# Optimization experiments

Hardware: AMD Instinct MI355X
Metric: run time of the kernel (lower is better)

Reference implementation:

```python
import jax, jax.numpy as jnp
import numpy as np

N = 50000        # nodes
E = 800000       # edges (avg degree 16)
IN_DIM = 256
H = 8            # heads
D = 32           # out_dim per head
T = 4            # edge_type_num
F = 16           # edge_feature_dim
NEG_SLOPE = 0.2


def setup_inputs() -> dict:
    key = jax.random.key(0)
    ks = jax.random.split(key, 9)
    feat = jax.random.normal(ks[0], (N, IN_DIM), dtype=jnp.float32)
    e_pro = jax.random.normal(ks[1], (E, F), dtype=jnp.float32)
    mask = jax.random.uniform(ks[2], (E, T), dtype=jnp.float32)
    W_n = jax.random.normal(ks[3], (IN_DIM, H * D), dtype=jnp.float32) * (1.0 / np.sqrt(IN_DIM))
    attn_l = jax.random.normal(ks[4], (H, D, T), dtype=jnp.float32) * 0.1
    attn_r = jax.random.normal(ks[5], (H, D, T), dtype=jnp.float32) * 0.1
    attn_m = jax.random.normal(ks[6], (H, F, T), dtype=jnp.float32) * 0.1
    src = jax.random.randint(ks[7], (E,), 0, N, dtype=jnp.int32)
    dst = jax.random.randint(ks[8], (E,), 0, N, dtype=jnp.int32)
    return {"feat": feat, "e_pro": e_pro, "mask": mask, "W_n": W_n,
            "attn_l": attn_l, "attn_r": attn_r, "attn_m": attn_m,
            "src": src, "dst": dst}


def reference(feat, e_pro, mask, W_n, attn_l, attn_r, attn_m, src, dst):
    # node projection: [N, H, D]
    feat_src = (feat @ W_n).reshape(N, H, D)

    # per-node attention logits per edge type: [N, H, T]
    el = jnp.einsum("nhd,hdt->nht", feat_src, attn_l)
    er = jnp.einsum("nhd,hdt->nht", feat_src, attn_r)
    # per-edge logits per edge type: [E, H, T]
    em = jnp.einsum("ef,hft->eht", e_pro, attn_m)

    # bmm with edge-type mask [E, T] -> scalar per head: [E, H]
    left = jnp.einsum("eht,et->eh", el[src], mask)
    right = jnp.einsum("eht,et->eh", er[dst], mask)
    em_e = jnp.einsum("eht,et->eh", em, mask)

    e = (left + right + em_e) / 3.0
    e = jnp.where(e > 0, e, NEG_SLOPE * e)  # leaky_relu

    # edge softmax over incoming edges of each dst node (stable)
    e_max = jax.ops.segment_max(e, dst, num_segments=N)          # [N, H]
    e_exp = jnp.exp(e - e_max[dst])                               # [E, H]
    e_sum = jax.ops.segment_sum(e_exp, dst, num_segments=N)      # [N, H]
    a = e_exp / e_sum[dst]                                       # [E, H]

    # u_mul_e + sum aggregation: [E, H, D] -> [N, H, D]
    msg = feat_src[src] * a[:, :, None]
    rst = jax.ops.segment_sum(msg, dst, num_segments=N)

    # cat=True: concat heads
    return rst.reshape(N, H * D)
```

## Files before the change

kernel.cpp:

```cpp
#include <hip/hip_runtime.h>
#include <hip/hip_bf16.h>
#include <hip/hip_fp16.h>

#define NN 50000
#define NEDGE 800000
#define INDIM 256
#define NH 8
#define ND 32
#define HD 256
#define NT 4
#define NF 16

typedef __attribute__((ext_vector_type(8))) short s16x8;
typedef __attribute__((ext_vector_type(4))) float f32x4;
typedef unsigned short u16;

__device__ __forceinline__ float bf2f(u16 u) {
    return __uint_as_float(((unsigned int)u) << 16);
}
__device__ __forceinline__ u16 f2bf(float f) {
    __hip_bfloat16 h = __float2bfloat16(f);
    return *reinterpret_cast<u16*>(&h);
}
__device__ __forceinline__ u16 f2h(float f) {
    __half h = __float2half(f);
    return *reinterpret_cast<u16*>(&h);
}
__device__ __forceinline__ float h2f(u16 u) {
    __half h = *reinterpret_cast<__half*>(&u);
    return __half2float(h);
}

__global__ __launch_bounds__(256) void wt_kernel(const float* __restrict__ W,
                                                 u16* __restrict__ Wt)
{
    int idx = blockIdx.x * 256 + threadIdx.x;
    int k = idx >> 8, c = idx & 255;
    Wt[(size_t)c * 256 + k] = f2bf(W[idx]);
}

__global__ __launch_bounds__(256) void gemm_mfma(
    const float* __restrict__ feat, const u16* __restrict__ Wt,
    u16* __restrict__ fs, int nrows)
{
    const int wave = threadIdx.x >> 6, lane = threadIdx.x & 63;
    const int brow = blockIdx.x * 32;
    const int c0 = wave * 64;
    const int rA = lane & 15;
    const int kg = lane >> 4;

    int r0 = brow + rA;
    int r1 = brow + 16 + rA;
    if (r0 >= nrows) r0 = nrows - 1;
    if (r1 >= nrows) r1 = nrows - 1;

    f32x4 acc[2][4] = {};

    for (int k0 = 0; k0 < 256; k0 += 32) {
        const int kk = k0 + kg * 8;
        const float* pa0 = feat + (size_t)r0 * 256 + kk;
        const float* pa1 = feat + (size_t)r1 * 256 + kk;
        float4 x0 = *reinterpret_cast<const float4*>(pa0);
        float4 x1 = *reinterpret_cast<const float4*>(pa0 + 4);
        float4 y0 = *reinterpret_cast<const float4*>(pa1);
        float4 y1 = *reinterpret_cast<const float4*>(pa1 + 4);
        s16x8 a0, a1;
        a0[0] = (short)f2bf(x0.x); a0[1] = (short)f2bf(x0.y);
        a0[2] = (short)f2bf(x0.z); a0[3] = (short)f2bf(x0.w);
        a0[4] = (short)f2bf(x1.x); a0[5] = (short)f2bf(x1.y);
        a0[6] = (short)f2bf(x1.z); a0[7] = (short)f2bf(x1.w);
        a1[0] = (short)f2bf(y0.x); a1[1] = (short)f2bf(y0.y);
        a1[2] = (short)f2bf(y0.z); a1[3] = (short)f2bf(y0.w);
        a1[4] = (short)f2bf(y1.x); a1[5] = (short)f2bf(y1.y);
        a1[6] = (short)f2bf(y1.z); a1[7] = (short)f2bf(y1.w);
        #pragma unroll
        for (int ct = 0; ct < 4; ++ct) {
            s16x8 b = *reinterpret_cast<const s16x8*>(Wt + (size_t)(c0 + ct * 16 + rA) * 256 + kk);
            acc[0][ct] = __builtin_amdgcn_mfma_f32_16x16x32_bf16(a0, b, acc[0][ct], 0, 0, 0);
            acc[1][ct] = __builtin_amdgcn_mfma_f32_16x16x32_bf16(a1, b, acc[1][ct], 0, 0, 0);
        }
    }

    #pragma unroll
    for (int rt = 0; rt < 2; ++rt) {
        #pragma unroll
        for (int r = 0; r < 4; ++r) {
            int row = brow + rt * 16 + kg * 4 + r;
            if (row < nrows) {
                #pragma unroll
                for (int ct = 0; ct < 4; ++ct) {
                    fs[(size_t)row * 256 + c0 + ct * 16 + rA] = f2bf(acc[rt][ct][r]);
                }
            }
        }
    }
}

__global__ __launch_bounds__(256) void elr_kernel(
    const u16* __restrict__ fs,
    const float* __restrict__ attn_l, const float* __restrict__ attn_r,
    u16* __restrict__ el, u16* __restrict__ er, int n)
{
    __shared__ float s_al[NH * ND * NT];
    __shared__ float s_ar[NH * ND * NT];
    for (int i = threadIdx.x; i < NH * ND * NT; i += 256) {
        s_al[i] = attn_l[i];
        s_ar[i] = attn_r[i];
    }
    __syncthreads();
    int wv = threadIdx.x >> 6, lane = threadIdx.x & 63;
    int node = blockIdx.x * 4 + wv;
    if (node >= n) return;
    int h = lane >> 3, j0 = (lane & 7) * 4;
    ushort4 u = *reinterpret_cast<const ushort4*>(fs + (size_t)node * HD + lane * 4);
    float f0 = bf2f(u.x), f1 = bf2f(u.y), f2 = bf2f(u.z), f3 = bf2f(u.w);
    const float* al = s_al + h * (ND * NT) + j0 * NT;
    const float* ar = s_ar + h * (ND * NT) + j0 * NT;
    float pl[NT], pr[NT];
    #pragma unroll
    for (int t = 0; t < NT; ++t) {
        pl[t] = f0*al[t] + f1*al[NT + t] + f2*al[2*NT + t] + f3*al[3*NT + t];
        pr[t] = f0*ar[t] + f1*ar[NT + t] + f2*ar[2*NT + t] + f3*ar[3*NT + t];
    }
    #pragma unroll
    for (int d = 1; d < 8; d <<= 1) {
        #pragma unroll
        for (int t = 0; t < NT; ++t) {
            pl[t] += __shfl_xor(pl[t], d);
            pr[t] += __shfl_xor(pr[t], d);
        }
    }
    if ((lane & 7) == 0) {
        ushort4 ol, orr;
        ol.x = f2h(pl[0]); ol.y = f2h(pl[1]); ol.z = f2h(pl[2]); ol.w = f2h(pl[3]);
        orr.x = f2h(pr[0]); orr.y = f2h(pr[1]); orr.z = f2h(pr[2]); orr.w = f2h(pr[3]);
        *reinterpret_cast<ushort4*>(el + (size_t)node * (NH*NT) + h * NT) = ol;
        *reinterpret_cast<ushort4*>(er + (size_t)node * (NH*NT) + h * NT) = orr;
    }
}

__global__ void init_kernel(int* cnt, int* cursor, int n) {
    int i = blockIdx.x * 256 + threadIdx.x;
    if (i < n) { cnt[i] = 0; cursor[i] = 0; }
}

__global__ void hist_kernel(const int* __restrict__ dst, int* __restrict__ cnt, int ne) {
    int e = blockIdx.x * 256 + threadIdx.x;
    if (e < ne) atomicAdd(&cnt[dst[e]], 1);
}

__global__ void scan1_kernel(const int* __restrict__ cnt, int* __restrict__ off,
                             int* __restrict__ blksum, int n) {
    __shared__ int sm[256];
    int i = blockIdx.x * 256 + threadIdx.x;
    int v = (i < n) ? cnt[i] : 0;
    sm[threadIdx.x] = v;
    __syncthreads();
    for (int d = 1; d < 256; d <<= 1) {
        int t = (threadIdx.x >= d) ? sm[threadIdx.x - d] : 0;
        __syncthreads();
        sm[threadIdx.x] += t;
        __syncthreads();
    }
    if (i < n) off[i] = sm[threadIdx.x] - v;
    if (threadIdx.x == 255) blksum[blockIdx.x] = sm[255];
}

__global__ void scan2_kernel(int* blksum, int nb) {
    __shared__ int sm[256];
    int v = (threadIdx.x < nb) ? blksum[threadIdx.x] : 0;
    sm[threadIdx.x] = v;
    __syncthreads();
    for (int d = 1; d < 256; d <<= 1) {
        int t = (threadIdx.x >= d) ? sm[threadIdx.x - d] : 0;
        __syncthreads();
        sm[threadIdx.x] += t;
        __syncthreads();
    }
    blksum[threadIdx.x] = sm[threadIdx.x] - v;
}

__global__ void scan3_kernel(int* __restrict__ off, const int* __restrict__ blksum,
                             int n, int ne) {
    int i = blockIdx.x * 256 + threadIdx.x;
    if (i < n) off[i] += blksum[blockIdx.x];
    if (i == 0) off[n] = ne;
}

__global__ __launch_bounds__(256) void edgefill_kernel(
    const float* __restrict__ e_pro, const float* __restrict__ mask,
    const float* __restrict__ attn_m,
    const int* __restrict__ src, const int* __restrict__ dst,
    const u16* __restrict__ el, const u16* __restrict__ er,
    const int* __restrict__ off, int* __restrict__ cursor,
    int* __restrict__ srcS, float* __restrict__ eS, int ne)
{
    __shared__ float s_amT[NF * NT * NH];
    for (int i = threadIdx.x; i < NH * NF * NT; i += 256) {
        int h = i >> 6, f = (i >> 2) & 15, t = i & 3;
        s_amT[(f * NT + t) * NH + h] = attn_m[i];
    }
    __syncthreads();

    int e = blockIdx.x * 32 + (threadIdx.x >> 3);
    if (e >= ne) return;
    const int lane = threadIdx.x & 63;
    const int j = threadIdx.x & 7;

    int s = src[e], d = dst[e];
    float4 mk = *reinterpret_cast<const float4*>(mask + (size_t)e * NT);

    union { uint2 v; u16 u[4]; } lv, rv;
    lv.v = *reinterpret_cast<const uint2*>(el + (size_t)s * (NH*NT) + j * NT);
    rv.v = *reinterpret_cast<const uint2*>(er + (size_t)d * (NH*NT) + j * NT);

    float epf[NF];
    #pragma unroll
    for (int q = 0; q < 4; ++q) {
        float4 v = *reinterpret_cast<const float4*>(e_pro + (size_t)e * NF + q * 4);
        epf[q*4+0] = v.x; epf[q*4+1] = v.y; epf[q*4+2] = v.z; epf[q*4+3] = v.w;
    }

    float em = 0.f;
    #pragma unroll
    for (int f = 0; f < NF; ++f) {
        float am = mk.x * s_amT[(f*NT + 0) * NH + j]
                 + mk.y * s_amT[(f*NT + 1) * NH + j]
                 + mk.z * s_amT[(f*NT + 2) * NH + j]
                 + mk.w * s_amT[(f*NT + 3) * NH + j];
        em = fmaf(epf[f], am, em);
    }
    float left  = mk.x*h2f(lv.u[0]) + mk.y*h2f(lv.u[1]) + mk.z*h2f(lv.u[2]) + mk.w*h2f(lv.u[3]);
    float right = mk.x*h2f(rv.u[0]) + mk.y*h2f(rv.u[1]) + mk.z*h2f(rv.u[2]) + mk.w*h2f(rv.u[3]);

    float val = (left + right + em) * (1.0f / 3.0f);
    val = val > 0.f ? val : 0.2f * val;

    int slot;
    if (j == 0) slot = off[d] + atomicAdd(&cursor[d], 1);
    slot = __shfl(slot, lane & 56);

    eS[(size_t)slot * NH + j] = val;
    if (j == 0) srcS[slot] = s;
}

__global__ __launch_bounds__(256) void agg_kernel(
    const int* __restrict__ off, const int* __restrict__ srcS,
    const float* __restrict__ eS, const u16* __restrict__ fs,
    float* __restrict__ out, int n)
{
    int wv = threadIdx.x >> 6, lane = threadIdx.x & 63;
    int node = blockIdx.x * 4 + wv;
    if (node >= n) return;
    int beg = off[node], end = off[node + 1];

    int h = lane & 7, sub = lane >> 3;
    float m = -INFINITY, s = 0.f;
    for (int i = beg + sub; i < end; i += 8) {
        float v = eS[(size_t)i * NH + h];
        if (v > m) { s = s * __expf(m - v) + 1.f; m = v; }
        else         s += __expf(v - m);
    }
    #pragma unroll
    for (int d = 8; d < 64; d <<= 1) {
        float mo = __shfl_xor(m, d);
        float so = __shfl_xor(s, d);
        if (mo > m)        { s = s * __expf(m - mo) + so; m = mo; }
        else if (so > 0.f)   s += so * __expf(mo - m);
    }

    int h2 = lane >> 3;
    float M = __shfl(m, h2);
    float S = __shfl(s, h2);
    float invS = S > 0.f ? 1.f / S : 0.f;
    const int col = lane * 4;
    float a0 = 0.f, a1 = 0.f, a2 = 0.f, a3 = 0.f;
    int i = beg;
    for (; i + 3 < end; i += 4) {
        int s0 = srcS[i], s1 = srcS[i+1], s2 = srcS[i+2], s3 = srcS[i+3];
        float w0 = __expf(eS[(size_t)(i  ) * NH + h2] - M) * invS;
        float w1 = __expf(eS[(size_t)(i+1) * NH + h2] - M) * invS;
        float w2 = __expf(eS[(size_t)(i+2) * NH + h2] - M) * invS;
        float w3 = __expf(eS[(size_t)(i+3) * NH + h2] - M) * invS;
        ushort4 u0 = *reinterpret_cast<const ushort4*>(fs + (size_t)s0 * HD + col);
        ushort4 u1 = *reinterpret_cast<const ushort4*>(fs + (size_t)s1 * HD + col);
        ushort4 u2 = *reinterpret_cast<const ushort4*>(fs + (size_t)s2 * HD + col);
        ushort4 u3 = *reinterpret_cast<const ushort4*>(fs + (size_t)s3 * HD + col);
        a0 = fmaf(w0, bf2f(u0.x), a0); a1 = fmaf(w0, bf2f(u0.y), a1);
        a2 = fmaf(w0, bf2f(u0.z), a2); a3 = fmaf(w0, bf2f(u0.w), a3);
        a0 = fmaf(w1, bf2f(u1.x), a0); a1 = fmaf(w1, bf2f(u1.y), a1);
        a2 = fmaf(w1, bf2f(u1.z), a2); a3 = fmaf(w1, bf2f(u1.w), a3);
        a0 = fmaf(w2, bf2f(u2.x), a0); a1 = fmaf(w2, bf2f(u2.y), a1);
        a2 = fmaf(w2, bf2f(u2.z), a2); a3 = fmaf(w2, bf2f(u2.w), a3);
        a0 = fmaf(w3, bf2f(u3.x), a0); a1 = fmaf(w3, bf2f(u3.y), a1);
        a2 = fmaf(w3, bf2f(u3.z), a2); a3 = fmaf(w3, bf2f(u3.w), a3);
    }
    for (; i < end; ++i) {
        int sn = srcS[i];
        float w = __expf(eS[(size_t)i * NH + h2] - M) * invS;
        ushort4 u = *reinterpret_cast<const ushort4*>(fs + (size_t)sn * HD + col);
        a0 = fmaf(w, bf2f(u.x), a0); a1 = fmaf(w, bf2f(u.y), a1);
        a2 = fmaf(w, bf2f(u.z), a2); a3 = fmaf(w, bf2f(u.w), a3);
    }
    *reinterpret_cast<float4*>(&out[(size_t)node * HD + col]) = make_float4(a0, a1, a2, a3);
}

extern "C" void kernel_launch(void* const* d_in, const int* in_sizes, int n_in,
                              void* d_out, int out_size, void* d_ws, size_t ws_size,
                              hipStream_t stream)
{
    const float* feat   = (const float*)d_in[0];
    const float* e_pro  = (const float*)d_in[1];
    const float* mask   = (const float*)d_in[2];
    const float* W_n    = (const float*)d_in[3];
    const float* attn_l = (const float*)d_in[4];
    const float* attn_r = (const float*)d_in[5];
    const float* attn_m = (const float*)d_in[6];
    const int* src      = (const int*)d_in[7];
    const int* dst      = (const int*)d_in[8];
    float* out = (float*)d_out;

    char* ws = (char*)d_ws;
    size_t o = 0;
    auto alloc = [&](size_t bytes) -> void* {
        void* p = (void*)(ws + o);
        o += (bytes + 255) & ~(size_t)255;
        return p;
    };
    u16* fs     = (u16*)alloc((size_t)NN * HD * 2);
    u16* Wt     = (u16*)alloc((size_t)INDIM * HD * 2);
    u16* el     = (u16*)alloc((size_t)NN * NH * NT * 2);
    u16* er     = (u16*)alloc((size_t)NN * NH * NT * 2);
    float* eS   = (float*)alloc((size_t)NEDGE * NH * 4);
    int* srcS   = (int*)alloc((size_t)NEDGE * 4);
    int* cnt    = (int*)alloc((size_t)NN * 4);
    int* cursor = (int*)alloc((size_t)NN * 4);
    int* offs   = (int*)alloc((size_t)(NN + 1) * 4);
    int* blksum = (int*)alloc(256 * 4);
    (void)ws_size; (void)in_sizes; (void)n_in; (void)out_size;

    dim3 b256(256);
    hipLaunchKernelGGL(wt_kernel, dim3(256), b256, 0, stream, W_n, Wt);
    hipLaunchKernelGGL(gemm_mfma, dim3((NN + 31) / 32), b256, 0, stream, feat, Wt, fs, NN);
    hipLaunchKernelGGL(elr_kernel, dim3((NN + 3) / 4), b256, 0, stream, fs, attn_l, attn_r, el, er, NN);
    hipLaunchKernelGGL(init_kernel, dim3((NN + 255) / 256), b256, 0, stream, cnt, cursor, NN);
    hipLaunchKernelGGL(hist_kernel, dim3((NEDGE + 255) / 256), b256, 0, stream, dst, cnt, NEDGE);
    hipLaunchKernelGGL(scan1_kernel, dim3((NN + 255) / 256), b256, 0, stream, cnt, offs, blksum, NN);
    hipLaunchKernelGGL(scan2_kernel, dim3(1), b256, 0, stream, blksum, (NN + 255) / 256);
    hipLaunchKernelGGL(scan3_kernel, dim3((NN + 255) / 256), b256, 0, stream, offs, blksum, NN, NEDGE);
    hipLaunchKernelGGL(edgefill_kernel, dim3((NEDGE + 31) / 32), b256, 0, stream,
                       e_pro, mask, attn_m, src, dst, el, er, offs, cursor, srcS, eS, NEDGE);
    hipLaunchKernelGGL(agg_kernel, dim3((NN + 3) / 4), b256, 0, stream, offs, srcS, eS, fs, out, NN);
}
```

Baseline: 270.3 us.

## Split edge scoring from CSR slot assignment and gather logits via edge index

Moves the atomic slot assignment into a separate thread-per-edge kernel that writes an edge-index permutation and sorted src. The edge scoring kernel now writes logits in original edge order with coalesced stores instead of scattered stores to sorted slots. The aggregation kernel gathers logits through the permutation. The shared-memory attn_m table is also repacked as float4 per (f,h) so each feature needs one LDS read. The cost is an extra kernel launch, an extra index array, and indirect, uncoalesced 32-byte gathers of logits in the aggregation's two passes.

```diff
diff --git a/kernel.cpp b/kernel.cpp
--- a/kernel.cpp
+++ b/kernel.cpp
@@ -187,24 +187,36 @@
     if (i == 0) off[n] = ne;
 }
 
-__global__ __launch_bounds__(256) void edgefill_kernel(
+__global__ void fillidx_kernel(const int* __restrict__ dst, const int* __restrict__ src,
+                               const int* __restrict__ off, int* __restrict__ cursor,
+                               int* __restrict__ eIdx, int* __restrict__ srcS, int ne) {
+    int e = blockIdx.x * 256 + threadIdx.x;
+    if (e < ne) {
+        int d = dst[e];
+        int p = atomicAdd(&cursor[d], 1);
+        int slot = off[d] + p;
+        eIdx[slot] = e;
+        srcS[slot] = src[e];
+    }
+}
+
+__global__ __launch_bounds__(256) void edge_kernel(
     const float* __restrict__ e_pro, const float* __restrict__ mask,
     const float* __restrict__ attn_m,
     const int* __restrict__ src, const int* __restrict__ dst,
     const u16* __restrict__ el, const u16* __restrict__ er,
-    const int* __restrict__ off, int* __restrict__ cursor,
-    int* __restrict__ srcS, float* __restrict__ eS, int ne)
-{
-    __shared__ float s_amT[NF * NT * NH];
-    for (int i = threadIdx.x; i < NH * NF * NT; i += 256) {
-        int h = i >> 6, f = (i >> 2) & 15, t = i & 3;
-        s_amT[(f * NT + t) * NH + h] = attn_m[i];
+    float* __restrict__ val, int ne)
+{
+    __shared__ float4 s_am4[NF][NH];
+    for (int i = threadIdx.x; i < NH * NF; i += 256) {
+        int h = i >> 4, f = i & 15;
+        const float* p = attn_m + (size_t)h * (NF * NT) + f * NT;
+        s_am4[f][h] = make_float4(p[0], p[1], p[2], p[3]);
     }
     __syncthreads();
 
     int e = blockIdx.x * 32 + (threadIdx.x >> 3);
     if (e >= ne) return;
-    const int lane = threadIdx.x & 63;
     const int j = threadIdx.x & 7;
 
     int s = src[e], d = dst[e];
@@ -224,30 +236,22 @@
     float em = 0.f;
     #pragma unroll
     for (int f = 0; f < NF; ++f) {
-        float am = mk.x * s_amT[(f*NT + 0) * NH + j]
-                 + mk.y * s_amT[(f*NT + 1) * NH + j]
-                 + mk.z * s_amT[(f*NT + 2) * NH + j]
-                 + mk.w * s_amT[(f*NT + 3) * NH + j];
-        em = fmaf(epf[f], am, em);
+        float4 am = s_am4[f][j];
+        float amm = mk.x*am.x + mk.y*am.y + mk.z*am.z + mk.w*am.w;
+        em = fmaf(epf[f], amm, em);
     }
     float left  = mk.x*h2f(lv.u[0]) + mk.y*h2f(lv.u[1]) + mk.z*h2f(lv.u[2]) + mk.w*h2f(lv.u[3]);
     float right = mk.x*h2f(rv.u[0]) + mk.y*h2f(rv.u[1]) + mk.z*h2f(rv.u[2]) + mk.w*h2f(rv.u[3]);
 
-    float val = (left + right + em) * (1.0f / 3.0f);
-    val = val > 0.f ? val : 0.2f * val;
-
-    int slot;
-    if (j == 0) slot = off[d] + atomicAdd(&cursor[d], 1);
-    slot = __shfl(slot, lane & 56);
-
-    eS[(size_t)slot * NH + j] = val;
-    if (j == 0) srcS[slot] = s;
+    float v = (left + right + em) * (1.0f / 3.0f);
+    v = v > 0.f ? v : 0.2f * v;
+    val[(size_t)e * NH + j] = v;
 }
 
 __global__ __launch_bounds__(256) void agg_kernel(
-    const int* __restrict__ off, const int* __restrict__ srcS,
-    const float* __restrict__ eS, const u16* __restrict__ fs,
-    float* __restrict__ out, int n)
+    const int* __restrict__ off, const int* __restrict__ eIdx,
+    const int* __restrict__ srcS, const float* __restrict__ val,
+    const u16* __restrict__ fs, float* __restrict__ out, int n)
 {
     int wv = threadIdx.x >> 6, lane = threadIdx.x & 63;
     int node = blockIdx.x * 4 + wv;
@@ -257,7 +261,8 @@
     int h = lane & 7, sub = lane >> 3;
     float m = -INFINITY, s = 0.f;
     for (int i = beg + sub; i < end; i += 8) {
-        float v = eS[(size_t)i * NH + h];
+        int e = eIdx[i];
+        float v = val[(size_t)e * NH + h];
         if (v > m) { s = s * __expf(m - v) + 1.f; m = v; }
         else         s += __expf(v - m);
     }
@@ -277,11 +282,12 @@
     float a0 = 0.f, a1 = 0.f, a2 = 0.f, a3 = 0.f;
     int i = beg;
     for (; i + 3 < end; i += 4) {
+        int e0 = eIdx[i], e1 = eIdx[i+1], e2 = eIdx[i+2], e3 = eIdx[i+3];
         int s0 = srcS[i], s1 = srcS[i+1], s2 = srcS[i+2], s3 = srcS[i+3];
-        float w0 = __expf(eS[(size_t)(i  ) * NH + h2] - M) * invS;
-        float w1 = __expf(eS[(size_t)(i+1) * NH + h2] - M) * invS;
-        float w2 = __expf(eS[(size_t)(i+2) * NH + h2] - M) * invS;
-        float w3 = __expf(eS[(size_t)(i+3) * NH + h2] - M) * invS;
+        float w0 = __expf(val[(size_t)e0 * NH + h2] - M) * invS;
+        float w1 = __expf(val[(size_t)e1 * NH + h2] - M) * invS;
+        float w2 = __expf(val[(size_t)e2 * NH + h2] - M) * invS;
+        float w3 = __expf(val[(size_t)e3 * NH + h2] - M) * invS;
         ushort4 u0 = *reinterpret_cast<const ushort4*>(fs + (size_t)s0 * HD + col);
         ushort4 u1 = *reinterpret_cast<const ushort4*>(fs + (size_t)s1 * HD + col);
         ushort4 u2 = *reinterpret_cast<const ushort4*>(fs + (size_t)s2 * HD + col);
@@ -296,8 +302,9 @@
         a2 = fmaf(w3, bf2f(u3.z), a2); a3 = fmaf(w3, bf2f(u3.w), a3);
     }
     for (; i < end; ++i) {
+        int e = eIdx[i];
         int sn = srcS[i];
-        float w = __expf(eS[(size_t)i * NH + h2] - M) * invS;
+        float w = __expf(val[(size_t)e * NH + h2] - M) * invS;
         ushort4 u = *reinterpret_cast<const ushort4*>(fs + (size_t)sn * HD + col);
         a0 = fmaf(w, bf2f(u.x), a0); a1 = fmaf(w, bf2f(u.y), a1);
         a2 = fmaf(w, bf2f(u.z), a2); a3 = fmaf(w, bf2f(u.w), a3);
@@ -331,7 +338,8 @@
     u16* Wt     = (u16*)alloc((size_t)INDIM * HD * 2);
     u16* el     = (u16*)alloc((size_t)NN * NH * NT * 2);
     u16* er     = (u16*)alloc((size_t)NN * NH * NT * 2);
-    float* eS   = (float*)alloc((size_t)NEDGE * NH * 4);
+    float* val  = (float*)alloc((size_t)NEDGE * NH * 4);
+    int* eIdx   = (int*)alloc((size_t)NEDGE * 4);
     int* srcS   = (int*)alloc((size_t)NEDGE * 4);
     int* cnt    = (int*)alloc((size_t)NN * 4);
     int* cursor = (int*)alloc((size_t)NN * 4);
@@ -348,7 +356,10 @@
     hipLaunchKernelGGL(scan1_kernel, dim3((NN + 255) / 256), b256, 0, stream, cnt, offs, blksum, NN);
     hipLaunchKernelGGL(scan2_kernel, dim3(1), b256, 0, stream, blksum, (NN + 255) / 256);
     hipLaunchKernelGGL(scan3_kernel, dim3((NN + 255) / 256), b256, 0, stream, offs, blksum, NN, NEDGE);
-    hipLaunchKernelGGL(edgefill_kernel, dim3((NEDGE + 31) / 32), b256, 0, stream,
-                       e_pro, mask, attn_m, src, dst, el, er, offs, cursor, srcS, eS, NEDGE);
-    hipLaunchKernelGGL(agg_kernel, dim3((NN + 3) / 4), b256, 0, stream, offs, srcS, eS, fs, out, NN);
-}
+    hipLaunchKernelGGL(fillidx_kernel, dim3((NEDGE + 255) / 256), b256, 0, stream,
+                       dst, src, offs, cursor, eIdx, srcS, NEDGE);
+    hipLaunchKernelGGL(edge_kernel, dim3((NEDGE + 31) / 32), b256, 0, stream,
+                       e_pro, mask, attn_m, src, dst, el, er, val, NEDGE);
+    hipLaunchKernelGGL(agg_kernel, dim3((NN + 3) / 4), b256, 0, stream,
+                       offs, eIdx, srcS, val, fs, out, NN);
+}
```

After: 299.7 us. 10.9% more time.
